# Kernel tuning notes

Hardware: AMD Instinct MI355X
Metric: run time of the kernel (lower is better)

Reference implementation:

```python
import jax, jax.numpy as jnp
import numpy as np

B, T, D = 4, 4096, 512
K = 8192  # codebook_size


def setup_inputs() -> dict:
    key = jax.random.key(0)
    k1, k2 = jax.random.split(key)
    x = jax.random.normal(k1, (B, T, D), dtype=jnp.float32)
    embed = jax.random.normal(k2, (K, D), dtype=jnp.float32)
    return {"x": x, "embed": embed}


def reference(x, embed):
    # preprocess: flatten all leading dims -> [N, D]
    shape = x.shape
    xf = x.reshape(-1, shape[-1])  # [N, D]
    # quantize: negative squared euclidean distance, argmax over codebook
    x_sq = jnp.sum(xf * xf, axis=1, keepdims=True)          # [N, 1]
    e_sq = jnp.sum(embed * embed, axis=1)[None, :]          # [1, K]
    dist = -(x_sq - 2.0 * (xf @ embed.T) + e_sq)            # [N, K]
    embed_ind = jnp.argmax(dist, axis=-1)                   # [N]
    embed_ind = embed_ind.reshape(shape[:-1])               # [B, T]
    quantize = embed[embed_ind]                             # [B, T, D]
    return (quantize, embed_ind)
```

## Files before the change

### kernel.cpp

```cpp
#include <hip/hip_runtime.h>
#include <cstddef>
#include <cstdint>

typedef unsigned short ushort_t;
typedef unsigned long long ull_t;
typedef __attribute__((ext_vector_type(8))) short short8;
typedef __attribute__((ext_vector_type(4))) float f32x4;

constexpr int D_ = 512, K_ = 8192, N_ = 16384;
constexpr float MARGIN = 0.75f;

__device__ __forceinline__ ushort_t f2bf(float f) {
  unsigned u = __float_as_uint(f);
  return (ushort_t)((u + 0x7FFFu + ((u >> 16) & 1u)) >> 16);
}
__device__ __forceinline__ unsigned flipf(float s) {
  unsigned u = __float_as_uint(s);
  return (u & 0x80000000u) ? ~u : (u | 0x80000000u);
}
__device__ __forceinline__ float unflipf(unsigned m) {
  unsigned u = (m & 0x80000000u) ? (m ^ 0x80000000u) : ~m;
  return __uint_as_float(u);
}
__device__ __forceinline__ ull_t umax64(ull_t a, ull_t b) { return a > b ? a : b; }
__device__ __forceinline__ ull_t umin64(ull_t a, ull_t b) { return a < b ? a : b; }

__device__ __forceinline__ void gld16(void* l, const void* g) {
  __builtin_amdgcn_global_load_lds((const __attribute__((address_space(1))) void*)g,
                                   (__attribute__((address_space(3))) void*)l, 16, 0, 0);
}

__global__ __launch_bounds__(256) void conv_all(const float* __restrict__ x,
                                                const float* __restrict__ e,
                                                char* __restrict__ xbt, char* __restrict__ ebt,
                                                float* __restrict__ ehs) {
  const int g = threadIdx.x & 15, rr = threadIdx.x >> 4;
  if ((int)blockIdx.x < 1024) {
    const int tile = blockIdx.x >> 3, rg = blockIdx.x & 7;
    const int r = rg * 16 + rr;
    const float4* src = (const float4*)(x + ((size_t)(tile * 128 + r)) * D_ + g * 32);
    float4 f[8];
#pragma unroll
    for (int q = 0; q < 8; ++q) f[q] = src[q];
    char* dbase = xbt + (size_t)tile * 131072 + g * 8192 + r * 16;
#pragma unroll
    for (int kq = 0; kq < 4; ++kq) {
      float4 a = f[kq * 2], b = f[kq * 2 + 1];
      short8 v;
      v[0] = (short)f2bf(a.x); v[1] = (short)f2bf(a.y); v[2] = (short)f2bf(a.z); v[3] = (short)f2bf(a.w);
      v[4] = (short)f2bf(b.x); v[5] = (short)f2bf(b.y); v[6] = (short)f2bf(b.z); v[7] = (short)f2bf(b.w);
      *(short8*)(dbase + kq * 2048) = v;
    }
  } else {
    const int bid = blockIdx.x - 1024;
    const int tile = bid >> 3, rg = bid & 7;
    const int r = rg * 16 + rr;
    const int col = tile * 128 + r;
    const float4* src = (const float4*)(e + (size_t)col * D_ + g * 32);
    float4 f[8];
    float ss = 0.f;
#pragma unroll
    for (int q = 0; q < 8; ++q) {
      f[q] = src[q];
      ss += f[q].x * f[q].x + f[q].y * f[q].y + f[q].z * f[q].z + f[q].w * f[q].w;
    }
    char* dbase = ebt + (size_t)tile * 131072 + g * 8192 + r * 16;
#pragma unroll
    for (int kq = 0; kq < 4; ++kq) {
      float4 a = f[kq * 2], b = f[kq * 2 + 1];
      short8 v;
      v[0] = (short)f2bf(a.x); v[1] = (short)f2bf(a.y); v[2] = (short)f2bf(a.z); v[3] = (short)f2bf(a.w);
      v[4] = (short)f2bf(b.x); v[5] = (short)f2bf(b.y); v[6] = (short)f2bf(b.z); v[7] = (short)f2bf(b.w);
      *(short8*)(dbase + kq * 2048) = v;
    }
#pragma unroll
    for (int m = 1; m < 16; m <<= 1) ss += __shfl_xor(ss, m);
    if (g == 0) ehs[col] = 0.5f * ss;
  }
}

__global__ __launch_bounds__(256, 3) void dist_mfma(const char* __restrict__ xbt,
                                                    const char* __restrict__ ebt,
                                                    const float* __restrict__ ehs,
                                                    ull_t* __restrict__ ppu,
                                                    float* __restrict__ pps2) {
  __shared__ alignas(16) char lds[32768];
  const int tid = threadIdx.x, w = tid >> 6, l = tid & 63;
  const int fid = blockIdx.x + blockIdx.y * 128;
  const int k8 = fid & 7, j = fid >> 3;
  const int by = k8 * 8 + (j & 7), bx = j >> 3;
  const int row0 = bx * 128, col0 = by * 128;
  const int wr = w >> 1, wc = w & 1;
  const char* xsrc = xbt + (size_t)bx * 131072;
  const char* esrc = ebt + (size_t)by * 131072;

#pragma unroll
  for (int i = 0; i < 2; ++i) {
    gld16(lds + w * 2048 + i * 1024, xsrc + w * 2048 + i * 1024 + l * 16);
    gld16(lds + 8192 + w * 2048 + i * 1024, esrc + w * 2048 + i * 1024 + l * 16);
  }
  __syncthreads();

  f32x4 acc[4][4] = {};
  for (int g = 0; g < 16; ++g) {
    char* cbase = lds + (g & 1) * 16384;
    if (g < 15) {
      char* nbase = lds + ((g + 1) & 1) * 16384;
#pragma unroll
      for (int i = 0; i < 2; ++i) {
        gld16(nbase + w * 2048 + i * 1024, xsrc + (g + 1) * 8192 + w * 2048 + i * 1024 + l * 16);
        gld16(nbase + 8192 + w * 2048 + i * 1024, esrc + (g + 1) * 8192 + w * 2048 + i * 1024 + l * 16);
      }
    }
    short8 a[4], b[4];
#pragma unroll
    for (int i = 0; i < 4; ++i)
      a[i] = *(const short8*)(cbase + (l >> 4) * 2048 + (wr * 64 + i * 16 + (l & 15)) * 16);
#pragma unroll
    for (int jj = 0; jj < 4; ++jj)
      b[jj] = *(const short8*)(cbase + 8192 + (l >> 4) * 2048 + (wc * 64 + jj * 16 + (l & 15)) * 16);
#pragma unroll
    for (int i = 0; i < 4; ++i)
#pragma unroll
      for (int jj = 0; jj < 4; ++jj)
        acc[i][jj] = __builtin_amdgcn_mfma_f32_16x16x32_bf16(a[i], b[jj], acc[i][jj], 0, 0, 0);
    __syncthreads();
  }

  float eh[4];
  unsigned ic[4];
#pragma unroll
  for (int jj = 0; jj < 4; ++jj) {
    int col = col0 + wc * 64 + jj * 16 + (l & 15);
    eh[jj] = ehs[col];
    ic[jj] = 0xFFFFFFFFu - (unsigned)col;
  }
#pragma unroll
  for (int i = 0; i < 4; ++i)
#pragma unroll
    for (int jj = 0; jj < 4; ++jj)
#pragma unroll
      for (int r = 0; r < 4; ++r)
        acc[i][jj][r] -= eh[jj];

  float mx[4][4];
#pragma unroll
  for (int i = 0; i < 4; ++i)
#pragma unroll
    for (int r = 0; r < 4; ++r)
      mx[i][r] = fmaxf(fmaxf(acc[i][0][r], acc[i][1][r]), fmaxf(acc[i][2][r], acc[i][3][r]));
#pragma unroll
  for (int m = 1; m < 16; m <<= 1)
#pragma unroll
    for (int i = 0; i < 4; ++i)
#pragma unroll
      for (int r = 0; r < 4; ++r)
        mx[i][r] = fmaxf(mx[i][r], __shfl_xor(mx[i][r], m));

  unsigned ii[4][4];
#pragma unroll
  for (int i = 0; i < 4; ++i)
#pragma unroll
    for (int r = 0; r < 4; ++r) {
      unsigned t0 = (acc[i][0][r] == mx[i][r]) ? ic[0] : 0u;
      unsigned t1 = (acc[i][1][r] == mx[i][r]) ? ic[1] : 0u;
      unsigned t2 = (acc[i][2][r] == mx[i][r]) ? ic[2] : 0u;
      unsigned t3 = (acc[i][3][r] == mx[i][r]) ? ic[3] : 0u;
      unsigned u01 = t0 > t1 ? t0 : t1, u23 = t2 > t3 ? t2 : t3;
      ii[i][r] = u01 > u23 ? u01 : u23;
    }
#pragma unroll
  for (int m = 1; m < 16; m <<= 1)
#pragma unroll
    for (int i = 0; i < 4; ++i)
#pragma unroll
      for (int r = 0; r < 4; ++r) {
        unsigned o = __shfl_xor(ii[i][r], m);
        ii[i][r] = ii[i][r] > o ? ii[i][r] : o;
      }

  float s2[4][4];
#pragma unroll
  for (int i = 0; i < 4; ++i)
#pragma unroll
    for (int r = 0; r < 4; ++r) {
      float t0 = (ic[0] == ii[i][r]) ? -3e38f : acc[i][0][r];
      float t1 = (ic[1] == ii[i][r]) ? -3e38f : acc[i][1][r];
      float t2 = (ic[2] == ii[i][r]) ? -3e38f : acc[i][2][r];
      float t3 = (ic[3] == ii[i][r]) ? -3e38f : acc[i][3][r];
      s2[i][r] = fmaxf(fmaxf(t0, t1), fmaxf(t2, t3));
    }
#pragma unroll
  for (int m = 1; m < 16; m <<= 1)
#pragma unroll
    for (int i = 0; i < 4; ++i)
#pragma unroll
      for (int r = 0; r < 4; ++r)
        s2[i][r] = fmaxf(s2[i][r], __shfl_xor(s2[i][r], m));

  const int c = l & 15, g16 = l >> 4;
  float fs1 = -3e38f, fs2 = -3e38f;
  unsigned fii = 0;
#pragma unroll
  for (int i = 0; i < 4; ++i) {
    if ((c >> 2) == i) {
      int rsel = c & 3;
      fs1 = (rsel == 0) ? mx[i][0] : (rsel == 1) ? mx[i][1] : (rsel == 2) ? mx[i][2] : mx[i][3];
      fii = (rsel == 0) ? ii[i][0] : (rsel == 1) ? ii[i][1] : (rsel == 2) ? ii[i][2] : ii[i][3];
      fs2 = (rsel == 0) ? s2[i][0] : (rsel == 1) ? s2[i][1] : (rsel == 2) ? s2[i][2] : s2[i][3];
    }
  }
  ull_t fp = ((ull_t)flipf(fs1) << 32) | fii;
  const int rib = wr * 64 + (c >> 2) * 16 + g16 * 4 + (c & 3);

  ull_t* lp = (ull_t*)lds;
  float* ls2 = (float*)(lds + 2048);
  lp[wc * 128 + rib] = fp; ls2[wc * 128 + rib] = fs2;
  __syncthreads();
  if (wc == 0) {
    ull_t op = lp[128 + rib];
    float os2 = ls2[128 + rib];
    ull_t lo = umin64(fp, op);
    fs2 = fmaxf(fmaxf(fs2, os2), unflipf((unsigned)(lo >> 32)));
    fp = umax64(fp, op);
    ppu[(size_t)(row0 + rib) * 64 + by] = fp;
    pps2[(size_t)(row0 + rib) * 64 + by] = fs2;
  }
}

__global__ __launch_bounds__(256) void finalize(const float* __restrict__ x,
                                                const float* __restrict__ embed,
                                                const float* __restrict__ ehs,
                                                const ull_t* __restrict__ ppu,
                                                const float* __restrict__ pps2,
                                                float* __restrict__ out) {
  const int row = (blockIdx.x * 256 + threadIdx.x) >> 6;
  const int l = threadIdx.x & 63;
  ull_t p = ppu[(size_t)row * 64 + l];
  float s2 = pps2[(size_t)row * 64 + l];
  ull_t gp = p;
#pragma unroll
  for (int m = 1; m < 64; m <<= 1) gp = umax64(gp, __shfl_xor(gp, m));
  float gs = unflipf((unsigned)(gp >> 32));
  float t = gs - MARGIN;
  bool cand = (unflipf((unsigned)(p >> 32)) >= t);
  bool ovf = (s2 >= t);
  ull_t b1 = __ballot(cand);
  ull_t b2 = __ballot(ovf);
  int idx;
  if (__popcll(b1) == 1 && b2 == 0ull) {
    idx = (int)(0xFFFFFFFFu - (unsigned)(gp & 0xFFFFFFFFu));
  } else {
    const float4* xr4 = (const float4*)(x + (size_t)row * D_ + l * 8);
    float4 xa = xr4[0], xc = xr4[1];
    ull_t best = 0ull;
    ull_t bb = b1;
    while (bb) {
      int b = (int)__builtin_ctzll(bb);
      bb &= bb - 1;
      ull_t pb = __shfl(p, b);
      int col = (int)(0xFFFFFFFFu - (unsigned)(pb & 0xFFFFFFFFu));
      const float4* er4 = (const float4*)(embed + (size_t)col * D_ + l * 8);
      float4 ea = er4[0], ec = er4[1];
      float s = xa.x * ea.x + xa.y * ea.y + xa.z * ea.z + xa.w * ea.w
              + xc.x * ec.x + xc.y * ec.y + xc.z * ec.z + xc.w * ec.w;
#pragma unroll
      for (int m = 1; m < 64; m <<= 1) s += __shfl_xor(s, m);
      s -= ehs[col];
      best = umax64(best, ((ull_t)flipf(s) << 32) | (0xFFFFFFFFu - (unsigned)col));
    }
    while (b2) {
      int b = (int)__builtin_ctzll(b2);
      b2 &= b2 - 1;
      int c0 = b * 128;
      const float* xr = x + (size_t)row * D_;
      const float* e0p = embed + (size_t)(c0 + l) * D_;
      const float* e1p = embed + (size_t)(c0 + 64 + l) * D_;
      float a0 = 0.f, a1 = 0.f;
      for (int d = 0; d < D_; d += 4) {
        float4 xv = *(const float4*)(xr + d);
        float4 v0 = *(const float4*)(e0p + d);
        float4 v1 = *(const float4*)(e1p + d);
        a0 = fmaf(v0.x, xv.x, fmaf(v0.y, xv.y, fmaf(v0.z, xv.z, fmaf(v0.w, xv.w, a0))));
        a1 = fmaf(v1.x, xv.x, fmaf(v1.y, xv.y, fmaf(v1.z, xv.z, fmaf(v1.w, xv.w, a1))));
      }
      float s0 = a0 - ehs[c0 + l];
      float s1 = a1 - ehs[c0 + 64 + l];
      ull_t p0 = ((ull_t)flipf(s0) << 32) | (0xFFFFFFFFu - (unsigned)(c0 + l));
      ull_t p1 = ((ull_t)flipf(s1) << 32) | (0xFFFFFFFFu - (unsigned)(c0 + 64 + l));
      ull_t pk = umax64(p0, p1);
#pragma unroll
      for (int m = 1; m < 64; m <<= 1) pk = umax64(pk, __shfl_xor(pk, m));
      best = umax64(best, pk);
    }
    idx = (int)(0xFFFFFFFFu - (unsigned)(best & 0xFFFFFFFFu));
  }
  const float4* src = (const float4*)(embed + (size_t)idx * D_);
  float4* dst = (float4*)(out + (size_t)row * D_);
  dst[l] = src[l];
  dst[l + 64] = src[l + 64];
  if (l == 0) out[(size_t)N_ * D_ + row] = (float)idx;
}

extern "C" void kernel_launch(void* const* d_in, const int* in_sizes, int n_in,
                              void* d_out, int out_size, void* d_ws, size_t ws_size,
                              hipStream_t stream) {
  const float* x = (const float*)d_in[0];
  const float* e = (const float*)d_in[1];
  float* out = (float*)d_out;

  char* ws = (char*)d_ws;
  char* xbt = ws;
  char* ebt = ws + 16777216;
  float* ehs = (float*)(ws + 25165824);
  ull_t* ppu = (ull_t*)(ws + 25198592);
  float* pps2 = (float*)(ws + 33587200);

  conv_all<<<1536, 256, 0, stream>>>(x, e, xbt, ebt, ehs);
  dist_mfma<<<dim3(128, 64), 256, 0, stream>>>(xbt, ebt, ehs, ppu, pps2);
  finalize<<<4096, 256, 0, stream>>>(x, e, ehs, ppu, pps2, out);
}
```

Before: 251.3 us.

## Enlarge distance GEMM tiles to 256x256 with 512-thread blocks

```diff
diff --git a/kernel.cpp b/kernel.cpp
--- a/kernel.cpp
+++ b/kernel.cpp
@@ -36,26 +36,22 @@
                                                 float* __restrict__ ehs) {
   const int g = threadIdx.x & 15, rr = threadIdx.x >> 4;
   if ((int)blockIdx.x < 1024) {
-    const int tile = blockIdx.x >> 3, rg = blockIdx.x & 7;
-    const int r = rg * 16 + rr;
-    const float4* src = (const float4*)(x + ((size_t)(tile * 128 + r)) * D_ + g * 32);
+    const int row = blockIdx.x * 16 + rr;
+    const float4* src = (const float4*)(x + (size_t)row * D_ + g * 32);
     float4 f[8];
 #pragma unroll
     for (int q = 0; q < 8; ++q) f[q] = src[q];
-    char* dbase = xbt + (size_t)tile * 131072 + g * 8192 + r * 16;
+    char* dbase = xbt + (size_t)(row >> 8) * 262144 + g * 16384 + (row & 255) * 16;
 #pragma unroll
     for (int kq = 0; kq < 4; ++kq) {
       float4 a = f[kq * 2], b = f[kq * 2 + 1];
       short8 v;
       v[0] = (short)f2bf(a.x); v[1] = (short)f2bf(a.y); v[2] = (short)f2bf(a.z); v[3] = (short)f2bf(a.w);
       v[4] = (short)f2bf(b.x); v[5] = (short)f2bf(b.y); v[6] = (short)f2bf(b.z); v[7] = (short)f2bf(b.w);
-      *(short8*)(dbase + kq * 2048) = v;
+      *(short8*)(dbase + kq * 4096) = v;
     }
   } else {
-    const int bid = blockIdx.x - 1024;
-    const int tile = bid >> 3, rg = bid & 7;
-    const int r = rg * 16 + rr;
-    const int col = tile * 128 + r;
+    const int col = (blockIdx.x - 1024) * 16 + rr;
     const float4* src = (const float4*)(e + (size_t)col * D_ + g * 32);
     float4 f[8];
     float ss = 0.f;
@@ -64,14 +60,14 @@
       f[q] = src[q];
       ss += f[q].x * f[q].x + f[q].y * f[q].y + f[q].z * f[q].z + f[q].w * f[q].w;
     }
-    char* dbase = ebt + (size_t)tile * 131072 + g * 8192 + r * 16;
+    char* dbase = ebt + (size_t)(col >> 8) * 262144 + g * 16384 + (col & 255) * 16;
 #pragma unroll
     for (int kq = 0; kq < 4; ++kq) {
       float4 a = f[kq * 2], b = f[kq * 2 + 1];
       short8 v;
       v[0] = (short)f2bf(a.x); v[1] = (short)f2bf(a.y); v[2] = (short)f2bf(a.z); v[3] = (short)f2bf(a.w);
       v[4] = (short)f2bf(b.x); v[5] = (short)f2bf(b.y); v[6] = (short)f2bf(b.z); v[7] = (short)f2bf(b.w);
-      *(short8*)(dbase + kq * 2048) = v;
+      *(short8*)(dbase + kq * 4096) = v;
     }
 #pragma unroll
     for (int m = 1; m < 16; m <<= 1) ss += __shfl_xor(ss, m);
@@ -79,48 +75,50 @@
   }
 }
 
-__global__ __launch_bounds__(256, 3) void dist_mfma(const char* __restrict__ xbt,
+__global__ __launch_bounds__(512, 2) void dist_mfma(const char* __restrict__ xbt,
                                                     const char* __restrict__ ebt,
                                                     const float* __restrict__ ehs,
                                                     ull_t* __restrict__ ppu,
                                                     float* __restrict__ pps2) {
-  __shared__ alignas(16) char lds[32768];
+  __shared__ alignas(16) char lds[65536];
   const int tid = threadIdx.x, w = tid >> 6, l = tid & 63;
-  const int fid = blockIdx.x + blockIdx.y * 128;
+  const int fid = blockIdx.x + blockIdx.y * 64;
   const int k8 = fid & 7, j = fid >> 3;
-  const int by = k8 * 8 + (j & 7), bx = j >> 3;
-  const int row0 = bx * 128, col0 = by * 128;
-  const int wr = w >> 1, wc = w & 1;
-  const char* xsrc = xbt + (size_t)bx * 131072;
-  const char* esrc = ebt + (size_t)by * 131072;
+  const int by = k8 * 4 + (j & 3), bx = j >> 2;
+  const int row0 = bx * 256, col0 = by * 256;
+  const int wr = w >> 2, wc = w & 3;
+  const char* xsrc = xbt + (size_t)bx * 262144;
+  const char* esrc = ebt + (size_t)by * 262144;
 
 #pragma unroll
   for (int i = 0; i < 2; ++i) {
-    gld16(lds + w * 2048 + i * 1024, xsrc + w * 2048 + i * 1024 + l * 16);
-    gld16(lds + 8192 + w * 2048 + i * 1024, esrc + w * 2048 + i * 1024 + l * 16);
+    gld16(lds + i * 8192 + w * 1024, xsrc + i * 8192 + w * 1024 + l * 16);
+    gld16(lds + 16384 + i * 8192 + w * 1024, esrc + i * 8192 + w * 1024 + l * 16);
   }
   __syncthreads();
 
-  f32x4 acc[4][4] = {};
-  for (int g = 0; g < 16; ++g) {
-    char* cbase = lds + (g & 1) * 16384;
-    if (g < 15) {
-      char* nbase = lds + ((g + 1) & 1) * 16384;
+  f32x4 acc[8][4] = {};
+  for (int s = 0; s < 16; ++s) {
+    char* Ab = lds + (s & 1) * 32768;
+    char* Bb = Ab + 16384;
+    if (s < 15) {
+      char* An = lds + ((s + 1) & 1) * 32768;
 #pragma unroll
       for (int i = 0; i < 2; ++i) {
-        gld16(nbase + w * 2048 + i * 1024, xsrc + (g + 1) * 8192 + w * 2048 + i * 1024 + l * 16);
-        gld16(nbase + 8192 + w * 2048 + i * 1024, esrc + (g + 1) * 8192 + w * 2048 + i * 1024 + l * 16);
+        gld16(An + i * 8192 + w * 1024, xsrc + (s + 1) * 16384 + i * 8192 + w * 1024 + l * 16);
+        gld16(An + 16384 + i * 8192 + w * 1024, esrc + (s + 1) * 16384 + i * 8192 + w * 1024 + l * 16);
       }
     }
-    short8 a[4], b[4];
-#pragma unroll
-    for (int i = 0; i < 4; ++i)
-      a[i] = *(const short8*)(cbase + (l >> 4) * 2048 + (wr * 64 + i * 16 + (l & 15)) * 16);
+    const int kq = (l >> 4) * 4096, lc = (l & 15) * 16;
+    short8 a[8], b[4];
+#pragma unroll
+    for (int i = 0; i < 8; ++i)
+      a[i] = *(const short8*)(Ab + kq + (wr * 128 + i * 16) * 16 + lc);
 #pragma unroll
     for (int jj = 0; jj < 4; ++jj)
-      b[jj] = *(const short8*)(cbase + 8192 + (l >> 4) * 2048 + (wc * 64 + jj * 16 + (l & 15)) * 16);
-#pragma unroll
-    for (int i = 0; i < 4; ++i)
+      b[jj] = *(const short8*)(Bb + kq + (wc * 64 + jj * 16) * 16 + lc);
+#pragma unroll
+    for (int i = 0; i < 8; ++i)
 #pragma unroll
       for (int jj = 0; jj < 4; ++jj)
         acc[i][jj] = __builtin_amdgcn_mfma_f32_16x16x32_bf16(a[i], b[jj], acc[i][jj], 0, 0, 0);
@@ -136,95 +134,88 @@
     ic[jj] = 0xFFFFFFFFu - (unsigned)col;
   }
 #pragma unroll
-  for (int i = 0; i < 4; ++i)
+  for (int i = 0; i < 8; ++i)
 #pragma unroll
     for (int jj = 0; jj < 4; ++jj)
 #pragma unroll
       for (int r = 0; r < 4; ++r)
         acc[i][jj][r] -= eh[jj];
 
-  float mx[4][4];
-#pragma unroll
-  for (int i = 0; i < 4; ++i)
+  const int c = l & 15, g16 = l >> 4;
+  ull_t fp0 = 0, fp1 = 0;
+  float fs20 = -3e38f, fs21 = -3e38f;
+#pragma unroll
+  for (int i = 0; i < 8; ++i) {
+    float mv[4]; unsigned iv[4]; float sv[4];
 #pragma unroll
     for (int r = 0; r < 4; ++r)
-      mx[i][r] = fmaxf(fmaxf(acc[i][0][r], acc[i][1][r]), fmaxf(acc[i][2][r], acc[i][3][r]));
-#pragma unroll
-  for (int m = 1; m < 16; m <<= 1)
-#pragma unroll
-    for (int i = 0; i < 4; ++i)
-#pragma unroll
-      for (int r = 0; r < 4; ++r)
-        mx[i][r] = fmaxf(mx[i][r], __shfl_xor(mx[i][r], m));
-
-  unsigned ii[4][4];
-#pragma unroll
-  for (int i = 0; i < 4; ++i)
+      mv[r] = fmaxf(fmaxf(acc[i][0][r], acc[i][1][r]), fmaxf(acc[i][2][r], acc[i][3][r]));
+#pragma unroll
+    for (int m = 1; m < 16; m <<= 1)
+#pragma unroll
+      for (int r = 0; r < 4; ++r) mv[r] = fmaxf(mv[r], __shfl_xor(mv[r], m));
 #pragma unroll
     for (int r = 0; r < 4; ++r) {
-      unsigned t0 = (acc[i][0][r] == mx[i][r]) ? ic[0] : 0u;
-      unsigned t1 = (acc[i][1][r] == mx[i][r]) ? ic[1] : 0u;
-      unsigned t2 = (acc[i][2][r] == mx[i][r]) ? ic[2] : 0u;
-      unsigned t3 = (acc[i][3][r] == mx[i][r]) ? ic[3] : 0u;
+      unsigned t0 = (acc[i][0][r] == mv[r]) ? ic[0] : 0u;
+      unsigned t1 = (acc[i][1][r] == mv[r]) ? ic[1] : 0u;
+      unsigned t2 = (acc[i][2][r] == mv[r]) ? ic[2] : 0u;
+      unsigned t3 = (acc[i][3][r] == mv[r]) ? ic[3] : 0u;
       unsigned u01 = t0 > t1 ? t0 : t1, u23 = t2 > t3 ? t2 : t3;
-      ii[i][r] = u01 > u23 ? u01 : u23;
-    }
-#pragma unroll
-  for (int m = 1; m < 16; m <<= 1)
-#pragma unroll
-    for (int i = 0; i < 4; ++i)
+      iv[r] = u01 > u23 ? u01 : u23;
+    }
+#pragma unroll
+    for (int m = 1; m < 16; m <<= 1)
 #pragma unroll
       for (int r = 0; r < 4; ++r) {
-        unsigned o = __shfl_xor(ii[i][r], m);
-        ii[i][r] = ii[i][r] > o ? ii[i][r] : o;
+        unsigned o = __shfl_xor(iv[r], m);
+        iv[r] = iv[r] > o ? iv[r] : o;
       }
-
-  float s2[4][4];
-#pragma unroll
-  for (int i = 0; i < 4; ++i)
 #pragma unroll
     for (int r = 0; r < 4; ++r) {
-      float t0 = (ic[0] == ii[i][r]) ? -3e38f : acc[i][0][r];
-      float t1 = (ic[1] == ii[i][r]) ? -3e38f : acc[i][1][r];
-      float t2 = (ic[2] == ii[i][r]) ? -3e38f : acc[i][2][r];
-      float t3 = (ic[3] == ii[i][r]) ? -3e38f : acc[i][3][r];
-      s2[i][r] = fmaxf(fmaxf(t0, t1), fmaxf(t2, t3));
-    }
-#pragma unroll
-  for (int m = 1; m < 16; m <<= 1)
-#pragma unroll
-    for (int i = 0; i < 4; ++i)
-#pragma unroll
-      for (int r = 0; r < 4; ++r)
-        s2[i][r] = fmaxf(s2[i][r], __shfl_xor(s2[i][r], m));
-
-  const int c = l & 15, g16 = l >> 4;
-  float fs1 = -3e38f, fs2 = -3e38f;
-  unsigned fii = 0;
-#pragma unroll
-  for (int i = 0; i < 4; ++i) {
-    if ((c >> 2) == i) {
-      int rsel = c & 3;
-      fs1 = (rsel == 0) ? mx[i][0] : (rsel == 1) ? mx[i][1] : (rsel == 2) ? mx[i][2] : mx[i][3];
-      fii = (rsel == 0) ? ii[i][0] : (rsel == 1) ? ii[i][1] : (rsel == 2) ? ii[i][2] : ii[i][3];
-      fs2 = (rsel == 0) ? s2[i][0] : (rsel == 1) ? s2[i][1] : (rsel == 2) ? s2[i][2] : s2[i][3];
-    }
-  }
-  ull_t fp = ((ull_t)flipf(fs1) << 32) | fii;
-  const int rib = wr * 64 + (c >> 2) * 16 + g16 * 4 + (c & 3);
+      float t0 = (ic[0] == iv[r]) ? -3e38f : acc[i][0][r];
+      float t1 = (ic[1] == iv[r]) ? -3e38f : acc[i][1][r];
+      float t2 = (ic[2] == iv[r]) ? -3e38f : acc[i][2][r];
+      float t3 = (ic[3] == iv[r]) ? -3e38f : acc[i][3][r];
+      sv[r] = fmaxf(fmaxf(t0, t1), fmaxf(t2, t3));
+    }
+#pragma unroll
+    for (int m = 1; m < 16; m <<= 1)
+#pragma unroll
+      for (int r = 0; r < 4; ++r) sv[r] = fmaxf(sv[r], __shfl_xor(sv[r], m));
+
+    if ((c >> 1) == i) {
+      const int rb = (c & 1) * 2;
+      float m0 = (rb == 0) ? mv[0] : mv[2];
+      float m1 = (rb == 0) ? mv[1] : mv[3];
+      unsigned i0 = (rb == 0) ? iv[0] : iv[2];
+      unsigned i1 = (rb == 0) ? iv[1] : iv[3];
+      float q0 = (rb == 0) ? sv[0] : sv[2];
+      float q1 = (rb == 0) ? sv[1] : sv[3];
+      fp0 = ((ull_t)flipf(m0) << 32) | i0; fs20 = q0;
+      fp1 = ((ull_t)flipf(m1) << 32) | i1; fs21 = q1;
+    }
+  }
+  const int iOwn = c >> 1;
+  const int rr0 = wr * 128 + iOwn * 16 + g16 * 4 + (c & 1) * 2;
 
   ull_t* lp = (ull_t*)lds;
-  float* ls2 = (float*)(lds + 2048);
-  lp[wc * 128 + rib] = fp; ls2[wc * 128 + rib] = fs2;
+  float* ls2 = (float*)(lds + 8192);
+  lp[wc * 256 + rr0] = fp0; lp[wc * 256 + rr0 + 1] = fp1;
+  ls2[wc * 256 + rr0] = fs20; ls2[wc * 256 + rr0 + 1] = fs21;
   __syncthreads();
-  if (wc == 0) {
-    ull_t op = lp[128 + rib];
-    float os2 = ls2[128 + rib];
-    ull_t lo = umin64(fp, op);
-    fs2 = fmaxf(fmaxf(fs2, os2), unflipf((unsigned)(lo >> 32)));
-    fp = umax64(fp, op);
-    ppu[(size_t)(row0 + rib) * 64 + by] = fp;
-    pps2[(size_t)(row0 + rib) * 64 + by] = fs2;
+  if (tid < 256) {
+    ull_t fpm = lp[tid];
+    float s2m = ls2[tid];
+#pragma unroll
+    for (int q = 1; q < 4; ++q) {
+      ull_t op = lp[q * 256 + tid];
+      float os2 = ls2[q * 256 + tid];
+      ull_t lo = umin64(fpm, op);
+      s2m = fmaxf(fmaxf(s2m, os2), unflipf((unsigned)(lo >> 32)));
+      fpm = umax64(fpm, op);
+    }
+    ppu[(size_t)(row0 + tid) * 32 + by] = fpm;
+    pps2[(size_t)(row0 + tid) * 32 + by] = s2m;
   }
 }
 
@@ -236,15 +227,17 @@
                                                 float* __restrict__ out) {
   const int row = (blockIdx.x * 256 + threadIdx.x) >> 6;
   const int l = threadIdx.x & 63;
-  ull_t p = ppu[(size_t)row * 64 + l];
-  float s2 = pps2[(size_t)row * 64 + l];
+  ull_t p = 0;
+  float s2 = -3e38f;
+  if (l < 32) { p = ppu[(size_t)row * 32 + l]; s2 = pps2[(size_t)row * 32 + l]; }
   ull_t gp = p;
 #pragma unroll
   for (int m = 1; m < 64; m <<= 1) gp = umax64(gp, __shfl_xor(gp, m));
   float gs = unflipf((unsigned)(gp >> 32));
   float t = gs - MARGIN;
-  bool cand = (unflipf((unsigned)(p >> 32)) >= t);
-  bool ovf = (s2 >= t);
+  float s1 = unflipf((unsigned)(p >> 32));
+  bool cand = (l < 32) && (s1 >= t);
+  bool ovf = (l < 32) && (s2 >= t);
   ull_t b1 = __ballot(cand);
   ull_t b2 = __ballot(ovf);
   int idx;
@@ -272,23 +265,28 @@
     while (b2) {
       int b = (int)__builtin_ctzll(b2);
       b2 &= b2 - 1;
-      int c0 = b * 128;
+      int c0 = b * 256;
       const float* xr = x + (size_t)row * D_;
       const float* e0p = embed + (size_t)(c0 + l) * D_;
       const float* e1p = embed + (size_t)(c0 + 64 + l) * D_;
-      float a0 = 0.f, a1 = 0.f;
+      const float* e2p = embed + (size_t)(c0 + 128 + l) * D_;
+      const float* e3p = embed + (size_t)(c0 + 192 + l) * D_;
+      float a0 = 0.f, a1 = 0.f, a2 = 0.f, a3 = 0.f;
       for (int d = 0; d < D_; d += 4) {
         float4 xv = *(const float4*)(xr + d);
         float4 v0 = *(const float4*)(e0p + d);
         float4 v1 = *(const float4*)(e1p + d);
+        float4 v2 = *(const float4*)(e2p + d);
+        float4 v3 = *(const float4*)(e3p + d);
         a0 = fmaf(v0.x, xv.x, fmaf(v0.y, xv.y, fmaf(v0.z, xv.z, fmaf(v0.w, xv.w, a0))));
         a1 = fmaf(v1.x, xv.x, fmaf(v1.y, xv.y, fmaf(v1.z, xv.z, fmaf(v1.w, xv.w, a1))));
+        a2 = fmaf(v2.x, xv.x, fmaf(v2.y, xv.y, fmaf(v2.z, xv.z, fmaf(v2.w, xv.w, a2))));
+        a3 = fmaf(v3.x, xv.x, fmaf(v3.y, xv.y, fmaf(v3.z, xv.z, fmaf(v3.w, xv.w, a3))));
       }
-      float s0 = a0 - ehs[c0 + l];
-      float s1 = a1 - ehs[c0 + 64 + l];
-      ull_t p0 = ((ull_t)flipf(s0) << 32) | (0xFFFFFFFFu - (unsigned)(c0 + l));
-      ull_t p1 = ((ull_t)flipf(s1) << 32) | (0xFFFFFFFFu - (unsigned)(c0 + 64 + l));
-      ull_t pk = umax64(p0, p1);
+      ull_t pk = ((ull_t)flipf(a0 - ehs[c0 + l]) << 32) | (0xFFFFFFFFu - (unsigned)(c0 + l));
+      pk = umax64(pk, ((ull_t)flipf(a1 - ehs[c0 + 64 + l]) << 32) | (0xFFFFFFFFu - (unsigned)(c0 + 64 + l)));
+      pk = umax64(pk, ((ull_t)flipf(a2 - ehs[c0 + 128 + l]) << 32) | (0xFFFFFFFFu - (unsigned)(c0 + 128 + l)));
+      pk = umax64(pk, ((ull_t)flipf(a3 - ehs[c0 + 192 + l]) << 32) | (0xFFFFFFFFu - (unsigned)(c0 + 192 + l)));
 #pragma unroll
       for (int m = 1; m < 64; m <<= 1) pk = umax64(pk, __shfl_xor(pk, m));
       best = umax64(best, pk);
@@ -314,9 +312,9 @@
   char* ebt = ws + 16777216;
   float* ehs = (float*)(ws + 25165824);
   ull_t* ppu = (ull_t*)(ws + 25198592);
-  float* pps2 = (float*)(ws + 33587200);
+  float* pps2 = (float*)(ws + 29392896);
 
   conv_all<<<1536, 256, 0, stream>>>(x, e, xbt, ebt, ehs);
-  dist_mfma<<<dim3(128, 64), 256, 0, stream>>>(xbt, ebt, ehs, ppu, pps2);
+  dist_mfma<<<dim3(64, 32), 512, 0, stream>>>(xbt, ebt, ehs, ppu, pps2);
   finalize<<<4096, 256, 0, stream>>>(x, e, ehs, ppu, pps2, out);
 }
```

Result: slower. 261.2 us (+3.9%).
